# Performance work log

Measured on AMD Instinct MI355X. Metric: run time of the kernel, lower is better.

The kernel has to match this reference:

```python
import jax, jax.numpy as jnp
import numpy as np

B, T, D_MODEL = 1, 2048, 4096
NUM_Q_HEADS, NUM_KV_HEADS, KEY_SIZE = 32, 8, 128
ATTN_MULT = 0.08838834764831845  # 1/sqrt(key_size)
MAX_ATTN_VAL = 30.0


def rotate_half(x):
    x1, x2 = jnp.split(x, 2, axis=-1)
    return jnp.concatenate((-x2, x1), axis=-1)


def apply_rope(x):
    # x: [b, t, h, d]; offset = 0, positions = arange(t)
    b, t, h, d = x.shape
    exponents = jnp.arange(0, d, 2, dtype=jnp.float32)
    inv_freq = 1.0 / (10000.0 ** (exponents / d))            # [d/2]
    pos = jnp.arange(t, dtype=jnp.float32)                   # [t]
    phase = pos[:, None] * inv_freq[None, :]                 # [t, d/2]
    phase = jnp.tile(phase, (1, 2))[None, :, None, :]        # [1, t, 1, d] (tiled, not interleaved)
    return (x * jnp.cos(phase) + rotate_half(x) * jnp.sin(phase)).astype(x.dtype)


def setup_inputs() -> dict:
    key = jax.random.key(0)
    ks = jax.random.split(key, 8)
    query = jax.random.normal(ks[0], (B, T, D_MODEL), dtype=jnp.float32)
    kk = jax.random.normal(ks[1], (B, T, D_MODEL), dtype=jnp.float32)
    vv = jax.random.normal(ks[2], (B, T, D_MODEL), dtype=jnp.float32)
    mask = jnp.tril(jnp.ones((T, T), dtype=bool))[None, None, :, :]  # causal [1,1,T,T]
    s = 0.02
    Wq = jax.random.normal(ks[3], (D_MODEL, NUM_Q_HEADS * KEY_SIZE), dtype=jnp.float32) * s
    Wk = jax.random.normal(ks[4], (D_MODEL, NUM_KV_HEADS * KEY_SIZE), dtype=jnp.float32) * s
    Wv = jax.random.normal(ks[5], (D_MODEL, NUM_KV_HEADS * KEY_SIZE), dtype=jnp.float32) * s
    Wo = jax.random.normal(ks[6], (NUM_Q_HEADS * KEY_SIZE, D_MODEL), dtype=jnp.float32) * s
    return {"query": query, "key": kk, "value": vv, "mask": mask,
            "Wq": Wq, "Wk": Wk, "Wv": Wv, "Wo": Wo}


def reference(query, key, value, mask, Wq, Wk, Wv, Wo):
    b, t, _ = query.shape
    d = KEY_SIZE
    h, kv_h = NUM_Q_HEADS, NUM_KV_HEADS
    g = h // kv_h
    # projections (no bias)
    q = (query @ Wq).reshape(b, t, h, d)
    k = (key @ Wk).reshape(b, t, kv_h, d)
    v = (value @ Wv).reshape(b, t, kv_h, d)
    # RoPE on q and k
    q = apply_rope(q)
    k = apply_rope(k)
    # GQA grouping: [b, t, kv_h, g, d]
    q = q.reshape(b, t, kv_h, g, d)
    logits = jnp.einsum('btkgd,bTkd->bkgtT', q, k).astype(jnp.float32)
    logits = logits * ATTN_MULT
    logits = MAX_ATTN_VAL * jnp.tanh(logits / MAX_ATTN_VAL)  # soft-capping
    m = mask[:, :, None, :, :]  # [b,1,1,t,T]
    logits = jnp.where(m, logits, -1e30)
    weights = jax.nn.softmax(logits, axis=-1).astype(query.dtype)
    attn = jnp.einsum('bkgtT,bTkd->btkgd', weights, v)
    attn = attn.reshape(b, t, h * d)
    return attn @ Wo
```

## Files before the change

kernel.cpp:

```cpp
#include <hip/hip_runtime.h>
#include <hip/hip_bf16.h>
#include <stdint.h>
#include <stddef.h>

#define T_SEQ 2048
#define DM    4096
#define NQH   32
#define NKVH  8
#define HD    128
#define ATTN_MULT 0.08838834764831845f

typedef __attribute__((ext_vector_type(8))) short bf16x8;
typedef __attribute__((ext_vector_type(4))) float f32x4;
typedef __attribute__((ext_vector_type(4))) unsigned int u32x4;

__device__ __forceinline__ unsigned short f2b(float f) {
  unsigned u = __builtin_bit_cast(unsigned, f);
  u = u + 0x7FFFu + ((u >> 16) & 1u);
  return (unsigned short)(u >> 16);
}
__device__ __forceinline__ float b2f(unsigned short h) {
  unsigned u = ((unsigned)h) << 16;
  return __builtin_bit_cast(float, u);
}

typedef const __attribute__((address_space(1))) void* gptr1_t;
typedef __attribute__((address_space(3))) void* lptr3_t;
__device__ __forceinline__ void gl_lds16(const void* g, void* l) {
  __builtin_amdgcn_global_load_lds((gptr1_t)g, (lptr3_t)l, 16, 0, 0);
}

#define MFMA16(a, b, c) __builtin_amdgcn_mfma_f32_16x16x32_bf16((a), (b), (c), 0, 0, 0)

__global__ __launch_bounds__(256) void transpose_cast4_kernel(
    const float* __restrict__ Wq, const float* __restrict__ Wk,
    const float* __restrict__ Wv, const float* __restrict__ Wo,
    unsigned short* __restrict__ WqT, unsigned short* __restrict__ WkT,
    unsigned short* __restrict__ WvT, unsigned short* __restrict__ WoT) {
  __shared__ float tile[64][65];
  int y = blockIdx.y;
  const float* W;
  unsigned short* WT;
  int N, n0;
  if (y < 64)      { W = Wq; WT = WqT; N = 4096; n0 = y * 64; }
  else if (y < 80) { W = Wk; WT = WkT; N = 1024; n0 = (y - 64) * 64; }
  else if (y < 96) { W = Wv; WT = WvT; N = 1024; n0 = (y - 80) * 64; }
  else             { W = Wo; WT = WoT; N = 4096; n0 = (y - 96) * 64; }
  const int K = 4096;
  int k0 = blockIdx.x * 64;
  int t = threadIdx.x;
  int rr = t >> 4;
  int cc = t & 15;
#pragma unroll
  for (int c = 0; c < 4; ++c) {
    int row = c * 16 + rr;
    float4 v = *(const float4*)&W[(size_t)(k0 + row) * N + n0 + cc * 4];
    tile[row][cc * 4 + 0] = v.x;
    tile[row][cc * 4 + 1] = v.y;
    tile[row][cc * 4 + 2] = v.z;
    tile[row][cc * 4 + 3] = v.w;
  }
  __syncthreads();
  int orow = t >> 2;
  int kb = (t & 3) * 16;
  u32x4 o1, o2;
#pragma unroll
  for (int u = 0; u < 4; ++u) {
    o1[u] = (unsigned)f2b(tile[kb + 2 * u][orow]) |
            ((unsigned)f2b(tile[kb + 2 * u + 1][orow]) << 16);
    o2[u] = (unsigned)f2b(tile[kb + 8 + 2 * u][orow]) |
            ((unsigned)f2b(tile[kb + 9 + 2 * u][orow]) << 16);
  }
  unsigned short* dst = &WT[(size_t)(n0 + orow) * K + k0 + kb];
  *(u32x4*)dst = o1;
  *(u32x4*)(dst + 8) = o2;
}

__global__ __launch_bounds__(256) void cast3_kernel(
    const float* __restrict__ a0, const float* __restrict__ a1, const float* __restrict__ a2,
    unsigned short* __restrict__ b0, unsigned short* __restrict__ b1, unsigned short* __restrict__ b2) {
  const float* in = blockIdx.z == 0 ? a0 : (blockIdx.z == 1 ? a1 : a2);
  unsigned short* out = blockIdx.z == 0 ? b0 : (blockIdx.z == 1 ? b1 : b2);
  size_t idx = ((size_t)blockIdx.x * 256 + threadIdx.x) * 8;
  float4 x = *(const float4*)(in + idx);
  float4 y = *(const float4*)(in + idx + 4);
  u32x4 v;
  v[0] = (unsigned)f2b(x.x) | ((unsigned)f2b(x.y) << 16);
  v[1] = (unsigned)f2b(x.z) | ((unsigned)f2b(x.w) << 16);
  v[2] = (unsigned)f2b(y.x) | ((unsigned)f2b(y.y) << 16);
  v[3] = (unsigned)f2b(y.z) | ((unsigned)f2b(y.w) << 16);
  *(u32x4*)(out + idx) = v;
}

template <bool F32OUT>
__device__ __forceinline__ void gemm256_body(
    unsigned short* lds,
    const unsigned short* __restrict__ A, const unsigned short* __restrict__ BT,
    void* __restrict__ C, int N, int Klen, int Kstride, int m0, int n0) {
  int t = threadIdx.x;
  int w = t >> 6, l = t & 63;
  int wm = w >> 2, wn = w & 3;
  int lr = l & 15, lh = l >> 4;

  f32x4 acc[8][4] = {};

  int scb = (((l & 7) ^ (l >> 3)) & 7) << 4;
  const int NT = Klen >> 6;
  int rswz = (lr & 7) << 4;
  int cb0 = (lh * 16) ^ rswz;
  int cb1 = (64 + lh * 16) ^ rswz;

  auto stageT = [&](const unsigned short* X, int base, int tt, int c, int ldsoff) {
#pragma unroll
    for (int h = 0; h < 2; ++h) {
      int grow = base + h * 128 + w * 8 + (l >> 3);
      const char* s1 = (const char*)X + ((size_t)grow * Kstride + tt * 64) * 2 + scb;
      gl_lds16(s1, (char*)lds + c * 65536 + ldsoff + h * 16384 + w * 1024);
      const char* s2 = (const char*)X + ((size_t)(grow + 64) * Kstride + tt * 64) * 2 + scb;
      gl_lds16(s2, (char*)lds + c * 65536 + ldsoff + h * 16384 + 8192 + w * 1024);
    }
  };

  stageT(A, m0, 0, 0, 0);
  stageT(BT, n0, 0, 0, 32768);
  asm volatile("s_waitcnt vmcnt(0)" ::: "memory");
  __builtin_amdgcn_s_barrier();

  for (int tt = 0; tt < NT; ++tt) {
    const char* Ab = (const char*)lds + (tt & 1) * 65536;
    const char* Bb = Ab + 32768;
    if (tt + 1 < NT) {
      int nb = (tt + 1) & 1;
      stageT(A, m0, tt + 1, nb, 0);
      stageT(BT, n0, tt + 1, nb, 32768);
    }
    int arow = wm * 128 + lr;
    int brow = wn * 64 + lr;
#pragma unroll
    for (int ks = 0; ks < 2; ++ks) {
      int cb = ks ? cb1 : cb0;
      bf16x8 av[8], bv[4];
#pragma unroll
      for (int i = 0; i < 8; ++i)
        av[i] = *(const bf16x8*)(Ab + (arow + i * 16) * 128 + cb);
#pragma unroll
      for (int j = 0; j < 4; ++j)
        bv[j] = *(const bf16x8*)(Bb + (brow + j * 16) * 128 + cb);
#pragma unroll
      for (int i = 0; i < 8; ++i)
#pragma unroll
        for (int j = 0; j < 4; ++j)
          acc[i][j] = MFMA16(av[i], bv[j], acc[i][j]);
    }
    asm volatile("s_waitcnt vmcnt(0)" ::: "memory");
    __builtin_amdgcn_s_barrier();
  }

#pragma unroll
  for (int i = 0; i < 8; ++i) {
#pragma unroll
    for (int j = 0; j < 4; ++j) {
#pragma unroll
      for (int r = 0; r < 4; ++r) {
        int row = m0 + wm * 128 + i * 16 + lh * 4 + r;
        int col = n0 + wn * 64 + j * 16 + lr;
        if constexpr (F32OUT)
          ((float*)C)[(size_t)row * N + col] = acc[i][j][r];
        else
          ((unsigned short*)C)[(size_t)row * N + col] = f2b(acc[i][j][r]);
      }
    }
  }
}

__global__ __launch_bounds__(512, 1) void qkv256_kernel(
    const unsigned short* __restrict__ qb, const unsigned short* __restrict__ WqT, unsigned short* __restrict__ Qp,
    const unsigned short* __restrict__ kb, const unsigned short* __restrict__ WkT, unsigned short* __restrict__ Kp,
    const unsigned short* __restrict__ vb, const unsigned short* __restrict__ WvT, unsigned short* __restrict__ Vp) {
  __shared__ unsigned short lds[2 * 32768];
  int flat = blockIdx.x;
  const unsigned short *A, *BT;
  unsigned short* C;
  int N, m0, n0;
  if (flat < 128) {
    A = qb; BT = WqT; C = Qp; N = NQH * HD;
    m0 = (flat >> 4) * 256;
    n0 = (flat & 15) * 256;
  } else {
    int lf = flat - 128;
    int sel = lf >> 5;
    int local = lf & 31;
    A = sel ? vb : kb;
    BT = sel ? WvT : WkT;
    C = sel ? Vp : Kp;
    N = NKVH * HD;
    m0 = (local >> 2) * 256;
    n0 = (local & 3) * 256;
  }
  gemm256_body<false>(lds, A, BT, C, N, DM, DM, m0, n0);
}

__global__ __launch_bounds__(512, 1) void oproj256_kernel(
    const unsigned short* __restrict__ A, const unsigned short* __restrict__ BT,
    float* __restrict__ P0, float* __restrict__ P1) {
  __shared__ unsigned short lds[2 * 32768];
  int flat = blockIdx.x;
  int ksl = flat >> 7;
  int local = flat & 127;
  int m0 = (local >> 4) * 256;
  int n0 = (local & 15) * 256;
  gemm256_body<true>(lds, A + ksl * 2048, BT + ksl * 2048,
                     ksl ? P1 : P0, DM, 2048, DM, m0, n0);
}

__global__ __launch_bounds__(256) void reduce_add_kernel(
    const float* __restrict__ P0, const float* __restrict__ P1, float* __restrict__ out) {
  size_t idx = ((size_t)blockIdx.x * 256 + threadIdx.x) * 4;
  float4 a = *(const float4*)(P0 + idx);
  float4 b = *(const float4*)(P1 + idx);
  float4 r;
  r.x = a.x + b.x; r.y = a.y + b.y; r.z = a.z + b.z; r.w = a.w + b.w;
  *(float4*)(out + idx) = r;
}

__global__ __launch_bounds__(256) void sincos_kernel(float2* __restrict__ tab) {
  int idx = blockIdx.x * 256 + threadIdx.x;
  int i = idx & 63;
  int tpos = idx >> 6;
  float invf = exp2f(-(float)i * (13.287712379549449f / 64.0f));
  float phase = (float)tpos * invf;
  float s, c;
  sincosf(phase, &s, &c);
  tab[idx] = make_float2(c, s);
}

__global__ __launch_bounds__(256) void rope_kernel(unsigned short* __restrict__ X,
                                                   const float2* __restrict__ tab,
                                                   int hshift, float scale) {
  int idx = blockIdx.x * 256 + threadIdx.x;
  int i = idx & 63;
  int rest = idx >> 6;
  int nheads = 1 << hshift;
  int hh = rest & (nheads - 1);
  int tpos = rest >> hshift;
  float2 cs = tab[tpos * 64 + i];
  size_t base = (size_t)tpos * ((size_t)nheads * HD) + (size_t)hh * HD + i;
  float x1 = b2f(X[base]);
  float x2 = b2f(X[base + 64]);
  X[base] = f2b((x1 * cs.x - x2 * cs.y) * scale);
  X[base + 64] = f2b((x2 * cs.x + x1 * cs.y) * scale);
}

__global__ __launch_bounds__(256) void vtrans_kernel(
    const unsigned short* __restrict__ V, unsigned short* __restrict__ VT) {
  size_t flat = ((size_t)blockIdx.x * 256 + threadIdx.x) * 8;
  int t8 = (int)(flat & (T_SEQ - 1));
  int dh = (int)(flat >> 11);
  u32x4 v;
#pragma unroll
  for (int u = 0; u < 4; ++u) {
    unsigned short lo = V[(size_t)(t8 + 2 * u) * (NKVH * HD) + dh];
    unsigned short hi = V[(size_t)(t8 + 2 * u + 1) * (NKVH * HD) + dh];
    v[u] = (unsigned)lo | ((unsigned)hi << 16);
  }
  *(u32x4*)(VT + flat) = v;
}

template <bool DIAG>
__device__ __forceinline__ void softmax_frag(const f32x4 s[4], float& lsum, bf16x8 pf[2],
                                             int lr, int lh, int wq) {
  constexpr float C2f = (float)(-60.0 * 1.4426950408889634);
  float pv[4][4];
#pragma unroll
  for (int ct = 0; ct < 4; ++ct)
#pragma unroll
    for (int r = 0; r < 4; ++r) {
      float u = exp2f(s[ct][r]);
      float p = exp2f(C2f * __builtin_amdgcn_rcpf(u + 1.0f));
      if constexpr (DIAG) {
        int kg = ct * 16 + lh * 4 + r;
        int qg = wq * 16 + lr;
        if (kg > qg) p = 0.0f;
      }
      pv[ct][r] = p;
      lsum += p;
    }
  unsigned pk[4][2];
#pragma unroll
  for (int ct = 0; ct < 4; ++ct) {
    pk[ct][0] = (unsigned)f2b(pv[ct][0]) | ((unsigned)f2b(pv[ct][1]) << 16);
    pk[ct][1] = (unsigned)f2b(pv[ct][2]) | ((unsigned)f2b(pv[ct][3]) << 16);
  }
  int s0 = ((lh & 1) << 5) + lr;
  int s1 = s0 + 16;
  bool hi = (lh >= 2);
#pragma unroll
  for (int ks = 0; ks < 2; ++ks) {
    unsigned a0 = (unsigned)__shfl((int)pk[2 * ks][0], s0, 64);
    unsigned a1 = (unsigned)__shfl((int)pk[2 * ks][1], s0, 64);
    unsigned a2 = (unsigned)__shfl((int)pk[2 * ks][0], s1, 64);
    unsigned a3 = (unsigned)__shfl((int)pk[2 * ks][1], s1, 64);
    unsigned b0 = (unsigned)__shfl((int)pk[2 * ks + 1][0], s0, 64);
    unsigned b1 = (unsigned)__shfl((int)pk[2 * ks + 1][1], s0, 64);
    unsigned b2 = (unsigned)__shfl((int)pk[2 * ks + 1][0], s1, 64);
    unsigned b3 = (unsigned)__shfl((int)pk[2 * ks + 1][1], s1, 64);
    u32x4 f;
    f[0] = hi ? b0 : a0;
    f[1] = hi ? b1 : a1;
    f[2] = hi ? b2 : a2;
    f[3] = hi ? b3 : a3;
    pf[ks] = __builtin_bit_cast(bf16x8, f);
  }
}

template <bool WITHA, bool DIAGA, bool DIAGB>
__device__ __forceinline__ void attn_tile(
    const char* KsCur, const char* VsCur,
    const bf16x8 qfA[4], const bf16x8 qfB[4],
    f32x4 oaccA[8], f32x4 oaccB[8],
    float& lsumA, float& lsumB,
    int lr, int lh, int wq) {
  f32x4 sB[4], sA[4];
#pragma unroll
  for (int ct = 0; ct < 4; ++ct) {
    f32x4 zB = {};
    f32x4 zA = {};
#pragma unroll
    for (int kk = 0; kk < 4; ++kk) {
      int row = ct * 16 + lr;
      int cb = (kk * 32 + lh * 8) * 2;
      bf16x8 kf = *(const bf16x8*)(KsCur + row * 256 + (cb ^ ((row & 7) << 4)));
      zB = MFMA16(kf, qfB[kk], zB);
      if constexpr (WITHA) zA = MFMA16(kf, qfA[kk], zA);
    }
    sB[ct] = zB;
    if constexpr (WITHA) sA[ct] = zA;
  }
  bf16x8 pfB[2], pfA[2];
  softmax_frag<DIAGB>(sB, lsumB, pfB, lr, lh, wq);
  if constexpr (WITHA) softmax_frag<DIAGA>(sA, lsumA, pfA, lr, lh, wq);
#pragma unroll
  for (int ks = 0; ks < 2; ++ks) {
    int pcb = (ks * 32 + lh * 8) * 2;
#pragma unroll
    for (int dt = 0; dt < 8; ++dt) {
      int vrow = dt * 16 + lr;
      bf16x8 vf = *(const bf16x8*)(VsCur + ((vrow * 128 + pcb) ^ ((vrow & 7) << 4)));
      oaccB[dt] = MFMA16(pfB[ks], vf, oaccB[dt]);
      if constexpr (WITHA) oaccA[dt] = MFMA16(pfA[ks], vf, oaccA[dt]);
    }
  }
}

__global__ __launch_bounds__(512, 2) void attn_kernel(
    const unsigned short* __restrict__ Q,
    const unsigned short* __restrict__ Kx,
    const unsigned short* __restrict__ VT,
    unsigned short* __restrict__ O) {
  __shared__ unsigned short Ks[2][64 * 128];
  __shared__ unsigned short Vs[2][128 * 64];

  int bx = blockIdx.x;
  int by = blockIdx.y;
  int qtA = bx, qtB = 31 - bx;
  int t = threadIdx.x;
  int w = t >> 6, l = t & 63;
  int wq = w & 3;
  int hh = by * 2 + (w >> 2);
  int kvh = by >> 1;
  int lr = l & 15, lh = l >> 4;

  bf16x8 qfA[4], qfB[4];
  {
    const unsigned short* qpA = Q + (size_t)(qtA * 64 + wq * 16 + lr) * (NQH * HD) + hh * HD + lh * 8;
    const unsigned short* qpB = Q + (size_t)(qtB * 64 + wq * 16 + lr) * (NQH * HD) + hh * HD + lh * 8;
#pragma unroll
    for (int kk = 0; kk < 4; ++kk) {
      qfA[kk] = *(const bf16x8*)(qpA + kk * 32);
      qfB[kk] = *(const bf16x8*)(qpB + kk * 32);
    }
  }

  f32x4 oaccA[8] = {}, oaccB[8] = {};
  float lsumA = 0.f, lsumB = 0.f;

  const char* KgB = (const char*)Kx + (size_t)kvh * HD * 2;
  const char* VgB = (const char*)VT + (size_t)kvh * HD * T_SEQ * 2;

  auto stage = [&](int kt, int b) {
#pragma unroll
    for (int c = 0; c < 2; ++c) {
      int chunk = w * 2 + c;
      int p = chunk * 1024 + l * 16;
      {
        int row = p >> 8;
        int cb = p & 255;
        int cbl = cb ^ ((row & 7) << 4);
        gl_lds16(KgB + (size_t)(kt * 64 + row) * (NKVH * HD * 2) + cbl,
                 (char*)Ks[b] + chunk * 1024);
      }
      {
        int row = p >> 7;
        int cb = p & 127;
        int cbl = cb ^ ((row & 7) << 4);
        gl_lds16(VgB + (size_t)row * (T_SEQ * 2) + (size_t)kt * 128 + cbl,
                 (char*)Vs[b] + chunk * 1024);
      }
    }
  };

  stage(0, 0);
  __syncthreads();

  int cur = 0;
  for (int kt = 0; kt <= qtB; ++kt) {
    if (kt < qtB) stage(kt + 1, cur ^ 1);
    const char* Kc = (const char*)Ks[cur];
    const char* Vc = (const char*)Vs[cur];
    if (kt < qtA)
      attn_tile<true, false, false>(Kc, Vc, qfA, qfB, oaccA, oaccB, lsumA, lsumB, lr, lh, wq);
    else if (kt == qtA)
      attn_tile<true, true, false>(Kc, Vc, qfA, qfB, oaccA, oaccB, lsumA, lsumB, lr, lh, wq);
    else if (kt < qtB)
      attn_tile<false, false, false>(Kc, Vc, qfA, qfB, oaccA, oaccB, lsumA, lsumB, lr, lh, wq);
    else
      attn_tile<false, false, true>(Kc, Vc, qfA, qfB, oaccA, oaccB, lsumA, lsumB, lr, lh, wq);
    __syncthreads();
    cur ^= 1;
  }

  lsumB += __shfl_xor(lsumB, 16, 64);
  lsumB += __shfl_xor(lsumB, 32, 64);
  lsumA += __shfl_xor(lsumA, 16, 64);
  lsumA += __shfl_xor(lsumA, 32, 64);

#pragma unroll
  for (int i = 0; i < 4; ++i) {
    int srcl = (l & 48) | (lh * 4 + i);
    float invB = 1.0f / __shfl(lsumB, srcl, 64);
    float invA = 1.0f / __shfl(lsumA, srcl, 64);
    int qgB = qtB * 64 + wq * 16 + lh * 4 + i;
    int qgA = qtA * 64 + wq * 16 + lh * 4 + i;
#pragma unroll
    for (int dt = 0; dt < 8; ++dt) {
      O[(size_t)qgB * (NQH * HD) + hh * HD + dt * 16 + lr] = f2b(oaccB[dt][i] * invB);
      O[(size_t)qgA * (NQH * HD) + hh * HD + dt * 16 + lr] = f2b(oaccA[dt][i] * invA);
    }
  }
}

extern "C" void kernel_launch(void* const* d_in, const int* in_sizes, int n_in,
                              void* d_out, int out_size, void* d_ws, size_t ws_size,
                              hipStream_t stream) {
  const float* query = (const float*)d_in[0];
  const float* key = (const float*)d_in[1];
  const float* value = (const float*)d_in[2];
  const float* Wq = (const float*)d_in[4];
  const float* Wk = (const float*)d_in[5];
  const float* Wv = (const float*)d_in[6];
  const float* Wo = (const float*)d_in[7];
  float* out = (float*)d_out;

  char* ws = (char*)d_ws;
  constexpr size_t OFF_WQT = 0;
  constexpr size_t OFF_WOT = 33554432;
  constexpr size_t OFF_WKT = 67108864;
  constexpr size_t OFF_WVT = 75497472;
  constexpr size_t OFF_QB = 83886080;
  constexpr size_t OFF_KB = 100663296;
  constexpr size_t OFF_VB = 117440512;
  constexpr size_t OFF_QP = 134217728;
  constexpr size_t OFF_KP = 150994944;
  constexpr size_t OFF_VP = 155189248;
  constexpr size_t OFF_VT = 159383552;
  constexpr size_t OFF_AT = 163577856;
  constexpr size_t WS_NEED = 180355072;
  if (ws_size < WS_NEED) return;

  unsigned short* WqT = (unsigned short*)(ws + OFF_WQT);
  unsigned short* WoT = (unsigned short*)(ws + OFF_WOT);
  unsigned short* WkT = (unsigned short*)(ws + OFF_WKT);
  unsigned short* WvT = (unsigned short*)(ws + OFF_WVT);
  unsigned short* qb = (unsigned short*)(ws + OFF_QB);
  unsigned short* kb = (unsigned short*)(ws + OFF_KB);
  unsigned short* vb = (unsigned short*)(ws + OFF_VB);
  unsigned short* Qp = (unsigned short*)(ws + OFF_QP);
  unsigned short* Kp = (unsigned short*)(ws + OFF_KP);
  unsigned short* Vp = (unsigned short*)(ws + OFF_VP);
  unsigned short* VTb = (unsigned short*)(ws + OFF_VT);
  unsigned short* attnb = (unsigned short*)(ws + OFF_AT);
  float2* tab = (float2*)(ws + OFF_QB);
  float* P0 = (float*)(ws + OFF_QB);
  float* P1 = (float*)(ws + OFF_VB);

  transpose_cast4_kernel<<<dim3(64, 160), 256, 0, stream>>>(
      Wq, Wk, Wv, Wo, WqT, WkT, WvT, WoT);
  cast3_kernel<<<dim3(4096, 1, 3), 256, 0, stream>>>(query, key, value, qb, kb, vb);
  qkv256_kernel<<<dim3(192), 512, 0, stream>>>(qb, WqT, Qp, kb, WkT, Kp, vb, WvT, Vp);
  sincos_kernel<<<dim3(T_SEQ * 64 / 256), 256, 0, stream>>>(tab);
  constexpr float C1 = (float)(0.08838834764831845 * 1.4426950408889634 / 15.0);
  rope_kernel<<<dim3(T_SEQ * NQH * 64 / 256), 256, 0, stream>>>(Qp, tab, 5, C1);
  rope_kernel<<<dim3(T_SEQ * NKVH * 64 / 256), 256, 0, stream>>>(Kp, tab, 3, 1.0f);
  vtrans_kernel<<<dim3(NKVH * HD * T_SEQ / (256 * 8)), 256, 0, stream>>>(Vp, VTb);
  attn_kernel<<<dim3(16, 16), 512, 0, stream>>>(Qp, Kp, VTb, attnb);
  oproj256_kernel<<<dim3(256), 512, 0, stream>>>(attnb, WoT, P0, P1);
  reduce_add_kernel<<<dim3(T_SEQ * DM / (256 * 4)), 256, 0, stream>>>(P0, P1, out);
}
```

Baseline: 380.6 us.

## Split paired-qtile attention blocks into single-tile blocks and tile V transpose via LDS

The attention kernel no longer pairs a short and a long causal query tile in one block. It launches 512 single-tile blocks, interleaving long and short tiles in the launch order, and raises launch bounds to 4 blocks per CU, aiming for more parallelism and occupancy with fewer registers per thread. The cost is that each K/V tile is now staged separately for each query tile rather than shared by two, roughly doubling K/V staging traffic. The V transpose now uses an LDS tile so global reads and writes are coalesced, replacing strided 2-byte gathers.

Measured after the change: 779.8 us. +104.9%, slower.

```diff
diff --git a/kernel.cpp b/kernel.cpp
--- a/kernel.cpp
+++ b/kernel.cpp
@@ -253,17 +253,31 @@
 
 __global__ __launch_bounds__(256) void vtrans_kernel(
     const unsigned short* __restrict__ V, unsigned short* __restrict__ VT) {
-  size_t flat = ((size_t)blockIdx.x * 256 + threadIdx.x) * 8;
-  int t8 = (int)(flat & (T_SEQ - 1));
-  int dh = (int)(flat >> 11);
-  u32x4 v;
-#pragma unroll
-  for (int u = 0; u < 4; ++u) {
-    unsigned short lo = V[(size_t)(t8 + 2 * u) * (NKVH * HD) + dh];
-    unsigned short hi = V[(size_t)(t8 + 2 * u + 1) * (NKVH * HD) + dh];
-    v[u] = (unsigned)lo | ((unsigned)hi << 16);
-  }
-  *(u32x4*)(VT + flat) = v;
+  __shared__ unsigned short tile[64][72];
+  int t0 = blockIdx.x * 64;
+  int dh0 = blockIdx.y * 64;
+  int tid = threadIdx.x;
+  int r = tid >> 3;
+  int c = (tid & 7) * 8;
+#pragma unroll
+  for (int p = 0; p < 2; ++p) {
+    int row = p * 32 + r;
+    bf16x8 v = *(const bf16x8*)&V[(size_t)(t0 + row) * (NKVH * HD) + dh0 + c];
+    *(bf16x8*)&tile[row][c] = v;
+  }
+  __syncthreads();
+#pragma unroll
+  for (int p = 0; p < 2; ++p) {
+    int dr = p * 32 + r;
+    u32x4 o;
+#pragma unroll
+    for (int u = 0; u < 4; ++u) {
+      unsigned short lo = tile[c + 2 * u][dr];
+      unsigned short hi = tile[c + 2 * u + 1][dr];
+      o[u] = (unsigned)lo | ((unsigned)hi << 16);
+    }
+    *(u32x4*)&VT[(size_t)(dh0 + dr) * T_SEQ + t0 + c] = o;
+  }
 }
 
 template <bool DIAG>
@@ -313,32 +327,25 @@
   }
 }
 
-template <bool WITHA, bool DIAGA, bool DIAGB>
-__device__ __forceinline__ void attn_tile(
-    const char* KsCur, const char* VsCur,
-    const bf16x8 qfA[4], const bf16x8 qfB[4],
-    f32x4 oaccA[8], f32x4 oaccB[8],
-    float& lsumA, float& lsumB,
-    int lr, int lh, int wq) {
-  f32x4 sB[4], sA[4];
+template <bool DIAG>
+__device__ __forceinline__ void attn_tile1(
+    const char* KsCur, const char* VsCur, const bf16x8 qf[4],
+    f32x4 oacc[8], float& lsum, int lr, int lh, int wq) {
+  f32x4 s[4];
 #pragma unroll
   for (int ct = 0; ct < 4; ++ct) {
-    f32x4 zB = {};
-    f32x4 zA = {};
+    f32x4 z = {};
 #pragma unroll
     for (int kk = 0; kk < 4; ++kk) {
       int row = ct * 16 + lr;
       int cb = (kk * 32 + lh * 8) * 2;
       bf16x8 kf = *(const bf16x8*)(KsCur + row * 256 + (cb ^ ((row & 7) << 4)));
-      zB = MFMA16(kf, qfB[kk], zB);
-      if constexpr (WITHA) zA = MFMA16(kf, qfA[kk], zA);
-    }
-    sB[ct] = zB;
-    if constexpr (WITHA) sA[ct] = zA;
-  }
-  bf16x8 pfB[2], pfA[2];
-  softmax_frag<DIAGB>(sB, lsumB, pfB, lr, lh, wq);
-  if constexpr (WITHA) softmax_frag<DIAGA>(sA, lsumA, pfA, lr, lh, wq);
+      z = MFMA16(kf, qf[kk], z);
+    }
+    s[ct] = z;
+  }
+  bf16x8 pf[2];
+  softmax_frag<DIAG>(s, lsum, pf, lr, lh, wq);
 #pragma unroll
   for (int ks = 0; ks < 2; ++ks) {
     int pcb = (ks * 32 + lh * 8) * 2;
@@ -346,13 +353,12 @@
     for (int dt = 0; dt < 8; ++dt) {
       int vrow = dt * 16 + lr;
       bf16x8 vf = *(const bf16x8*)(VsCur + ((vrow * 128 + pcb) ^ ((vrow & 7) << 4)));
-      oaccB[dt] = MFMA16(pfB[ks], vf, oaccB[dt]);
-      if constexpr (WITHA) oaccA[dt] = MFMA16(pfA[ks], vf, oaccA[dt]);
-    }
-  }
-}
-
-__global__ __launch_bounds__(512, 2) void attn_kernel(
+      oacc[dt] = MFMA16(pf[ks], vf, oacc[dt]);
+    }
+  }
+}
+
+__global__ __launch_bounds__(512, 4) void attn_kernel(
     const unsigned short* __restrict__ Q,
     const unsigned short* __restrict__ Kx,
     const unsigned short* __restrict__ VT,
@@ -361,28 +367,24 @@
   __shared__ unsigned short Vs[2][128 * 64];
 
   int bx = blockIdx.x;
-  int by = blockIdx.y;
-  int qtA = bx, qtB = 31 - bx;
+  int qt = (bx & 1) ? (bx >> 5) : (31 - (bx >> 5));
+  int hp = (bx >> 1) & 15;
   int t = threadIdx.x;
   int w = t >> 6, l = t & 63;
   int wq = w & 3;
-  int hh = by * 2 + (w >> 2);
-  int kvh = by >> 1;
+  int hh = hp * 2 + (w >> 2);
+  int kvh = hp >> 1;
   int lr = l & 15, lh = l >> 4;
 
-  bf16x8 qfA[4], qfB[4];
+  bf16x8 qf[4];
   {
-    const unsigned short* qpA = Q + (size_t)(qtA * 64 + wq * 16 + lr) * (NQH * HD) + hh * HD + lh * 8;
-    const unsigned short* qpB = Q + (size_t)(qtB * 64 + wq * 16 + lr) * (NQH * HD) + hh * HD + lh * 8;
-#pragma unroll
-    for (int kk = 0; kk < 4; ++kk) {
-      qfA[kk] = *(const bf16x8*)(qpA + kk * 32);
-      qfB[kk] = *(const bf16x8*)(qpB + kk * 32);
-    }
-  }
-
-  f32x4 oaccA[8] = {}, oaccB[8] = {};
-  float lsumA = 0.f, lsumB = 0.f;
+    const unsigned short* qp = Q + (size_t)(qt * 64 + wq * 16 + lr) * (NQH * HD) + hh * HD + lh * 8;
+#pragma unroll
+    for (int kk = 0; kk < 4; ++kk) qf[kk] = *(const bf16x8*)(qp + kk * 32);
+  }
+
+  f32x4 oacc[8] = {};
+  float lsum = 0.f;
 
   const char* KgB = (const char*)Kx + (size_t)kvh * HD * 2;
   const char* VgB = (const char*)VT + (size_t)kvh * HD * T_SEQ * 2;
@@ -413,39 +415,29 @@
   __syncthreads();
 
   int cur = 0;
-  for (int kt = 0; kt <= qtB; ++kt) {
-    if (kt < qtB) stage(kt + 1, cur ^ 1);
+  for (int kt = 0; kt <= qt; ++kt) {
+    if (kt < qt) stage(kt + 1, cur ^ 1);
     const char* Kc = (const char*)Ks[cur];
     const char* Vc = (const char*)Vs[cur];
-    if (kt < qtA)
-      attn_tile<true, false, false>(Kc, Vc, qfA, qfB, oaccA, oaccB, lsumA, lsumB, lr, lh, wq);
-    else if (kt == qtA)
-      attn_tile<true, true, false>(Kc, Vc, qfA, qfB, oaccA, oaccB, lsumA, lsumB, lr, lh, wq);
-    else if (kt < qtB)
-      attn_tile<false, false, false>(Kc, Vc, qfA, qfB, oaccA, oaccB, lsumA, lsumB, lr, lh, wq);
+    if (kt < qt)
+      attn_tile1<false>(Kc, Vc, qf, oacc, lsum, lr, lh, wq);
     else
-      attn_tile<false, false, true>(Kc, Vc, qfA, qfB, oaccA, oaccB, lsumA, lsumB, lr, lh, wq);
+      attn_tile1<true>(Kc, Vc, qf, oacc, lsum, lr, lh, wq);
     __syncthreads();
     cur ^= 1;
   }
 
-  lsumB += __shfl_xor(lsumB, 16, 64);
-  lsumB += __shfl_xor(lsumB, 32, 64);
-  lsumA += __shfl_xor(lsumA, 16, 64);
-  lsumA += __shfl_xor(lsumA, 32, 64);
+  lsum += __shfl_xor(lsum, 16, 64);
+  lsum += __shfl_xor(lsum, 32, 64);
 
 #pragma unroll
   for (int i = 0; i < 4; ++i) {
     int srcl = (l & 48) | (lh * 4 + i);
-    float invB = 1.0f / __shfl(lsumB, srcl, 64);
-    float invA = 1.0f / __shfl(lsumA, srcl, 64);
-    int qgB = qtB * 64 + wq * 16 + lh * 4 + i;
-    int qgA = qtA * 64 + wq * 16 + lh * 4 + i;
-#pragma unroll
-    for (int dt = 0; dt < 8; ++dt) {
-      O[(size_t)qgB * (NQH * HD) + hh * HD + dt * 16 + lr] = f2b(oaccB[dt][i] * invB);
-      O[(size_t)qgA * (NQH * HD) + hh * HD + dt * 16 + lr] = f2b(oaccA[dt][i] * invA);
-    }
+    float inv = 1.0f / __shfl(lsum, srcl, 64);
+    int qg = qt * 64 + wq * 16 + lh * 4 + i;
+#pragma unroll
+    for (int dt = 0; dt < 8; ++dt)
+      O[(size_t)qg * (NQH * HD) + hh * HD + dt * 16 + lr] = f2b(oacc[dt][i] * inv);
   }
 }
 
@@ -501,8 +493,8 @@
   constexpr float C1 = (float)(0.08838834764831845 * 1.4426950408889634 / 15.0);
   rope_kernel<<<dim3(T_SEQ * NQH * 64 / 256), 256, 0, stream>>>(Qp, tab, 5, C1);
   rope_kernel<<<dim3(T_SEQ * NKVH * 64 / 256), 256, 0, stream>>>(Kp, tab, 3, 1.0f);
-  vtrans_kernel<<<dim3(NKVH * HD * T_SEQ / (256 * 8)), 256, 0, stream>>>(Vp, VTb);
-  attn_kernel<<<dim3(16, 16), 512, 0, stream>>>(Qp, Kp, VTb, attnb);
+  vtrans_kernel<<<dim3(T_SEQ / 64, NKVH * HD / 64), 256, 0, stream>>>(Vp, VTb);
+  attn_kernel<<<dim3(512), 512, 0, stream>>>(Qp, Kp, VTb, attnb);
   oproj256_kernel<<<dim3(256), 512, 0, stream>>>(attnb, WoT, P0, P1);
   reduce_add_kernel<<<dim3(T_SEQ * DM / (256 * 4)), 256, 0, stream>>>(P0, P1, out);
 }
```
